# Kernel tuning notes

Hardware: AMD Instinct MI355X
Metric: run time of the kernel (lower is better)

Reference implementation:

```python
import jax, jax.numpy as jnp
import numpy as np

D_MODEL, D_STATE, D_CONV, EXPAND = 1024, 128, 4, 2
D_INNER = D_MODEL * EXPAND
PROJ_DIM = 2 * D_INNER + 2 * D_STATE + 1
CLIP = 8.0
EPS = 1e-5


def setup_inputs() -> dict:
    key = jax.random.key(0)
    ks = jax.random.split(key, 4)
    B, T = 4, 4096
    x = jax.random.normal(ks[0], (B, T, D_MODEL), dtype=jnp.float32)
    in_proj_w = jax.random.normal(ks[1], (PROJ_DIM, D_MODEL), dtype=jnp.float32) / np.sqrt(D_MODEL)
    conv_w = jax.random.normal(ks[2], (D_INNER, 1, D_CONV), dtype=jnp.float32) / np.sqrt(D_CONV)
    A_log = jnp.log(jnp.arange(1, D_STATE + 1, dtype=jnp.float32))
    Dp = jnp.ones((D_INNER,), jnp.float32)
    norm_w = jnp.ones((D_INNER,), jnp.float32)
    out_proj_w = jax.random.normal(ks[3], (D_MODEL, D_INNER), dtype=jnp.float32) / np.sqrt(D_INNER)
    return {"x": x, "in_proj_w": in_proj_w, "conv_w": conv_w, "A_log": A_log,
            "Dp": Dp, "norm_w": norm_w, "out_proj_w": out_proj_w}


def _csilu(v):
    return jnp.minimum(jax.nn.silu(v), CLIP)


def reference(x, in_proj_w, conv_w, A_log, Dp, norm_w, out_proj_w):
    B, T, _ = x.shape
    zxbcdt = x @ in_proj_w.T                                  # (B,T,PROJ_DIM)
    z = zxbcdt[..., :D_INNER]
    xm = zxbcdt[..., D_INNER:2 * D_INNER]
    Bp = zxbcdt[..., 2 * D_INNER:2 * D_INNER + D_STATE]
    Cp = zxbcdt[..., 2 * D_INNER + D_STATE:2 * D_INNER + 2 * D_STATE]
    dt = zxbcdt[..., -1]                                      # (B,T)

    xm = _csilu(xm)
    # causal depthwise conv1d (left pad d_conv-1, valid conv)
    xc = jnp.swapaxes(xm, 1, 2)                               # (B,D_INNER,T)
    xc = jnp.pad(xc, ((0, 0), (0, 0), (D_CONV - 1, 0)))
    xc = jax.lax.conv_general_dilated(
        xc, conv_w, window_strides=(1,), padding='VALID',
        dimension_numbers=('NCH', 'OIH', 'NCH'), feature_group_count=D_INNER)
    xm = _csilu(jnp.swapaxes(xc, 1, 2))                       # (B,T,D_INNER)

    A = -jnp.exp(A_log)                                       # (S,)
    dts = jax.nn.softplus(dt)                                 # (B,T)
    A_bar = jnp.exp(A[None, None, :] * dts[:, :, None])       # (B,T,S)
    B_bar = Bp * dts[:, :, None]                              # (B,T,S)

    h0 = jnp.zeros((B, D_INNER, D_STATE), x.dtype)

    def step(h, inp):
        a, b, c, xt = inp                                     # a,b,c:(B,S)  xt:(B,D_INNER)
        h = a[:, None, :] * h + b[:, None, :] * xt[:, :, None]
        y = jnp.einsum('bds,bs->bd', h, c) + Dp * xt
        return h, y

    xs = (jnp.swapaxes(A_bar, 0, 1), jnp.swapaxes(B_bar, 0, 1),
          jnp.swapaxes(Cp, 0, 1), jnp.swapaxes(xm, 0, 1))
    hT, ys = jax.lax.scan(step, h0, xs)
    y = jnp.swapaxes(ys, 0, 1)                                # (B,T,D_INNER)

    # RMSNorm then gate
    y = y * jax.lax.rsqrt(jnp.mean(y * y, axis=-1, keepdims=True) + EPS) * norm_w
    y = y * _csilu(z)
    out = y @ out_proj_w.T                                    # (B,T,D_MODEL)
    return out, jax.lax.stop_gradient(hT)
```

## Files before the change

kernel.cpp:

```cpp
#include <hip/hip_runtime.h>
#include <hip/hip_bf16.h>
#include <math.h>
#include <stdint.h>

#define D_MODEL 1024
#define D_STATE 128
#define D_INNER 2048
#define NCOLS   4352
#define NB      4
#define TLEN    4096
#define BT      16384
#define LCH     512
#define NCH     8

using bf16 = __hip_bfloat16;
typedef __attribute__((ext_vector_type(2))) float f32x2;
typedef __attribute__((ext_vector_type(4))) float f32x4;
typedef __attribute__((ext_vector_type(8))) short short8x;

__device__ __forceinline__ float csilu_fast(float v) {
    float e = __expf(-v);
    float s = v * __builtin_amdgcn_rcpf(1.f + e);
    return fminf(s, 8.f);
}

__device__ __forceinline__ void gload_lds16(const void* g, void* l) {
    __builtin_amdgcn_global_load_lds(
        (const __attribute__((address_space(1))) void*)g,
        (__attribute__((address_space(3))) void*)l, 16, 0, 0);
}

__global__ __launch_bounds__(256) void cast_kernel(const float* __restrict__ src,
                                                   bf16* __restrict__ dst, int n4) {
    int i = blockIdx.x * 256 + threadIdx.x;
    if (i < n4) {
        float4 v = ((const float4*)src)[i];
        dst[i*4+0] = __float2bfloat16(v.x);
        dst[i*4+1] = __float2bfloat16(v.y);
        dst[i*4+2] = __float2bfloat16(v.z);
        dst[i*4+3] = __float2bfloat16(v.w);
    }
}

__global__ __launch_bounds__(256) void split_kernel(const float* __restrict__ src,
                                                    bf16* __restrict__ hi,
                                                    bf16* __restrict__ lo, int n4) {
    int i = blockIdx.x * 256 + threadIdx.x;
    if (i < n4) {
        float4 v = ((const float4*)src)[i];
        #pragma unroll
        for (int j = 0; j < 4; ++j) {
            float f = (&v.x)[j];
            bf16 h = __float2bfloat16(f);
            hi[i*4+j] = h;
            lo[i*4+j] = __float2bfloat16(f - __bfloat162float(h));
        }
    }
}

__global__ __launch_bounds__(256) void gemm1_split(const bf16* __restrict__ Ah,
                                                   const bf16* __restrict__ Al,
                                                   const bf16* __restrict__ Bh,
                                                   const bf16* __restrict__ Bl,
                                                   bf16* __restrict__ zdst,
                                                   float* __restrict__ xmdst,
                                                   float* __restrict__ bcdst) {
    const int K = D_MODEL;
    __shared__ __align__(16) bf16 sAh[128*32], sAl[128*32];
    __shared__ __align__(16) bf16 sBh[128*32], sBl[128*32];
    const int tid  = threadIdx.x;
    const int lane = tid & 63;
    const int wave = tid >> 6;
    const int wr   = (wave >> 1) * 64;
    const int wc   = (wave & 1) * 64;
    const long arow0 = (long)blockIdx.x * 128;
    const long brow0 = (long)blockIdx.y * 128;
    const long kb = (long)K * 2;
    const bool prec = (blockIdx.y >= 16);
    const char* gAh = (const char*)Ah;
    const char* gAl = (const char*)Al;
    const char* gBh = (const char*)Bh;
    const char* gBl = (const char*)Bl;

    f32x4 acc[4][4] = {};
    const int c1 = tid, c2 = tid + 256;
    const long aoff1 = (arow0 + (c1 >> 2)) * kb + (c1 & 3) * 16;
    const long aoff2 = (arow0 + (c2 >> 2)) * kb + (c2 & 3) * 16;
    const long boff1 = (brow0 + (c1 >> 2)) * kb + (c1 & 3) * 16;
    const long boff2 = (brow0 + (c2 >> 2)) * kb + (c2 & 3) * 16;

    for (int k0 = 0; k0 < K; k0 += 32) {
        __syncthreads();
        const long kk = (long)k0 * 2;
        gload_lds16(gAh + aoff1 + kk, (char*)sAh + c1*16);
        gload_lds16(gAh + aoff2 + kk, (char*)sAh + c2*16);
        gload_lds16(gBh + boff1 + kk, (char*)sBh + c1*16);
        gload_lds16(gBh + boff2 + kk, (char*)sBh + c2*16);
        if (prec) {
            gload_lds16(gAl + aoff1 + kk, (char*)sAl + c1*16);
            gload_lds16(gAl + aoff2 + kk, (char*)sAl + c2*16);
            gload_lds16(gBl + boff1 + kk, (char*)sBl + c1*16);
            gload_lds16(gBl + boff2 + kk, (char*)sBl + c2*16);
        }
        __syncthreads();

        const int r    = lane & 15;
        const int koff = (lane >> 4) * 8;
        short8x ah[4], bh[4];
        #pragma unroll
        for (int m = 0; m < 4; ++m)
            ah[m] = *(const short8x*)(sAh + (wr + m*16 + r) * 32 + koff);
        #pragma unroll
        for (int n = 0; n < 4; ++n)
            bh[n] = *(const short8x*)(sBh + (wc + n*16 + r) * 32 + koff);
        if (prec) {
            short8x al[4], bl[4];
            #pragma unroll
            for (int m = 0; m < 4; ++m)
                al[m] = *(const short8x*)(sAl + (wr + m*16 + r) * 32 + koff);
            #pragma unroll
            for (int n = 0; n < 4; ++n)
                bl[n] = *(const short8x*)(sBl + (wc + n*16 + r) * 32 + koff);
            #pragma unroll
            for (int m = 0; m < 4; ++m)
                #pragma unroll
                for (int n = 0; n < 4; ++n) {
                    acc[m][n] = __builtin_amdgcn_mfma_f32_16x16x32_bf16(ah[m], bh[n], acc[m][n], 0, 0, 0);
                    acc[m][n] = __builtin_amdgcn_mfma_f32_16x16x32_bf16(ah[m], bl[n], acc[m][n], 0, 0, 0);
                    acc[m][n] = __builtin_amdgcn_mfma_f32_16x16x32_bf16(al[m], bh[n], acc[m][n], 0, 0, 0);
                }
        } else {
            #pragma unroll
            for (int m = 0; m < 4; ++m)
                #pragma unroll
                for (int n = 0; n < 4; ++n)
                    acc[m][n] = __builtin_amdgcn_mfma_f32_16x16x32_bf16(ah[m], bh[n], acc[m][n], 0, 0, 0);
        }
    }

    const int r4 = (lane >> 4) * 4;
    const int cl = lane & 15;
    if (blockIdx.y < 16) {
        #pragma unroll
        for (int m = 0; m < 4; ++m)
            #pragma unroll
            for (int n = 0; n < 4; ++n) {
                const long row = arow0 + wr + m*16 + r4;
                const long col = brow0 + wc + n*16 + cl;
                #pragma unroll
                for (int j = 0; j < 4; ++j)
                    zdst[(row + j) * 2048 + col] = __float2bfloat16(acc[m][n][j]);
            }
    } else if (blockIdx.y < 32) {
        #pragma unroll
        for (int m = 0; m < 4; ++m)
            #pragma unroll
            for (int n = 0; n < 4; ++n) {
                const long row = arow0 + wr + m*16 + r4;
                const long col = brow0 - 2048 + wc + n*16 + cl;
                #pragma unroll
                for (int j = 0; j < 4; ++j)
                    xmdst[(row + j) * 2048 + col] = acc[m][n][j];
            }
    } else {
        #pragma unroll
        for (int m = 0; m < 4; ++m)
            #pragma unroll
            for (int n = 0; n < 4; ++n) {
                const long row = arow0 + wr + m*16 + r4;
                const long col = brow0 - 4096 + wc + n*16 + cl;
                #pragma unroll
                for (int j = 0; j < 4; ++j)
                    bcdst[(row + j) * 256 + col] = acc[m][n][j];
            }
    }
}

__global__ __launch_bounds__(256) void gemm2_mfma(const bf16* __restrict__ A,
                                                  const bf16* __restrict__ B,
                                                  float* __restrict__ C) {
    const int K = D_INNER;
    __shared__ __align__(16) bf16 sA[128*32];
    __shared__ __align__(16) bf16 sB[128*32];
    const int tid  = threadIdx.x;
    const int lane = tid & 63;
    const int wave = tid >> 6;
    const int wr   = (wave >> 1) * 64;
    const int wc   = (wave & 1) * 64;
    const long arow0 = (long)blockIdx.x * 128;
    const long brow0 = (long)blockIdx.y * 128;
    const long kb = (long)K * 2;
    const char* gA = (const char*)A;
    const char* gB = (const char*)B;

    f32x4 acc[4][4] = {};
    const int c1 = tid, c2 = tid + 256;
    for (int k0 = 0; k0 < K; k0 += 32) {
        __syncthreads();
        gload_lds16(gA + (arow0 + (c1 >> 2)) * kb + k0*2 + (c1 & 3) * 16, (char*)sA + c1*16);
        gload_lds16(gA + (arow0 + (c2 >> 2)) * kb + k0*2 + (c2 & 3) * 16, (char*)sA + c2*16);
        gload_lds16(gB + (brow0 + (c1 >> 2)) * kb + k0*2 + (c1 & 3) * 16, (char*)sB + c1*16);
        gload_lds16(gB + (brow0 + (c2 >> 2)) * kb + k0*2 + (c2 & 3) * 16, (char*)sB + c2*16);
        __syncthreads();

        const int r    = lane & 15;
        const int koff = (lane >> 4) * 8;
        short8x af[4], bfr[4];
        #pragma unroll
        for (int m = 0; m < 4; ++m)
            af[m] = *(const short8x*)(sA + (wr + m*16 + r) * 32 + koff);
        #pragma unroll
        for (int n = 0; n < 4; ++n)
            bfr[n] = *(const short8x*)(sB + (wc + n*16 + r) * 32 + koff);
        #pragma unroll
        for (int m = 0; m < 4; ++m)
            #pragma unroll
            for (int n = 0; n < 4; ++n)
                acc[m][n] = __builtin_amdgcn_mfma_f32_16x16x32_bf16(af[m], bfr[n], acc[m][n], 0, 0, 0);
    }

    const int r4 = (lane >> 4) * 4;
    const int cl = lane & 15;
    #pragma unroll
    for (int m = 0; m < 4; ++m) {
        #pragma unroll
        for (int n = 0; n < 4; ++n) {
            const long row = arow0 + wr + m*16 + r4;
            const long col = brow0 + wc + n*16 + cl;
            #pragma unroll
            for (int j = 0; j < 4; ++j)
                C[(row + j) * D_MODEL + col] = acc[m][n][j];
        }
    }
}

__global__ __launch_bounds__(256) void dt_gemv(const float* __restrict__ x,
                                               const float* __restrict__ wdt,
                                               float* __restrict__ dts) {
    const int row  = blockIdx.x * 4 + (threadIdx.x >> 6);
    const int lane = threadIdx.x & 63;
    const float4* xr = (const float4*)(x + (long)row * D_MODEL);
    const float4* wr = (const float4*)wdt;
    float acc = 0.f;
    for (int i = lane; i < D_MODEL/4; i += 64) {
        float4 a = xr[i], b = wr[i];
        acc += a.x*b.x + a.y*b.y + a.z*b.z + a.w*b.w;
    }
    for (int o = 32; o > 0; o >>= 1) acc += __shfl_down(acc, o);
    if (lane == 0)
        dts[row] = fmaxf(acc, 0.f) + log1pf(expf(-fabsf(acc)));
}

__global__ __launch_bounds__(LCH) void cumsum_chunks(const float* __restrict__ dts,
                                                     float* __restrict__ cumdt) {
    __shared__ float s[LCH];
    const int t = threadIdx.x;
    const long base = (long)blockIdx.x * LCH;
    s[t] = dts[base + t];
    __syncthreads();
    for (int o = 1; o < LCH; o <<= 1) {
        float v = (t >= o) ? s[t - o] : 0.f;
        __syncthreads();
        s[t] += v;
        __syncthreads();
    }
    cumdt[base + t] = s[t];
}

__global__ __launch_bounds__(256) void scan_local(const float* __restrict__ dts,
                                                  const float* __restrict__ bc,
                                                  const float* __restrict__ A_log,
                                                  const float* __restrict__ xm,
                                                  const float* __restrict__ cw,
                                                  const float* __restrict__ Dp,
                                                  bf16* __restrict__ ybuf,
                                                  float* __restrict__ hbuf) {
    const int tid = threadIdx.x;
    const int dl  = tid & 63;
    const int q   = tid >> 6;
    const int d0  = blockIdx.x * 128 + dl;
    const int d1  = d0 + 64;
    const int ch  = blockIdx.y;
    const int b   = blockIdx.z;
    const long row0 = (long)b * TLEN + ch * LCH;
    const int s0   = q * 32;
    const int scol = dl & 31;
    const int half = dl >> 5;
    const int sg   = s0 + scol;
    const float As_l = -expf(A_log[sg]);

    const float w00 = cw[d0*4+0], w01 = cw[d0*4+1], w02 = cw[d0*4+2], w03 = cw[d0*4+3];
    const float w10 = cw[d1*4+0], w11 = cw[d1*4+1], w12 = cw[d1*4+2], w13 = cw[d1*4+3];
    const float dpv0 = Dp[d0], dpv1 = Dp[d1];

    float p00 = 0.f, p01 = 0.f, p02 = 0.f;
    float p10 = 0.f, p11 = 0.f, p12 = 0.f;
    if (ch != 0) {
        p00 = csilu_fast(xm[(row0 - 3) * 2048 + d0]);
        p01 = csilu_fast(xm[(row0 - 2) * 2048 + d0]);
        p02 = csilu_fast(xm[(row0 - 1) * 2048 + d0]);
        p10 = csilu_fast(xm[(row0 - 3) * 2048 + d1]);
        p11 = csilu_fast(xm[(row0 - 2) * 2048 + d1]);
        p12 = csilu_fast(xm[(row0 - 1) * 2048 + d1]);
    }

    f32x2 hA[16], hB[16];
    #pragma unroll
    for (int k = 0; k < 16; ++k) { hA[k] = (f32x2){0.f,0.f}; hB[k] = (f32x2){0.f,0.f}; }

    __shared__ __align__(16) float sa[8][128], sb[8][128], sc[8][128];
    __shared__ __align__(16) f32x2 yred[2][8][4][64];
    int pbuf = 0;

    float pfDT[4], pfB[4], pfC[4], pfXM0[8], pfXM1[8];
    #pragma unroll
    for (int k = 0; k < 4; ++k) {
        const long row = row0 + half + k*2;
        pfDT[k] = dts[row];
        pfB[k]  = bc[row*256 + sg];
        pfC[k]  = bc[row*256 + 128 + sg];
    }
    #pragma unroll
    for (int r = 0; r < 8; ++r) {
        pfXM0[r] = xm[(row0 + r) * 2048 + d0];
        pfXM1[r] = xm[(row0 + r) * 2048 + d1];
    }

    for (int tt = 0; tt < LCH; tt += 8) {
        #pragma unroll
        for (int k = 0; k < 4; ++k) {
            const int r = half + k*2;
            sa[r][sg] = __expf(As_l * pfDT[k]);
            sb[r][sg] = pfB[k] * pfDT[k];
            sc[r][sg] = pfC[k];
        }
        float curXM0[8], curXM1[8];
        #pragma unroll
        for (int r = 0; r < 8; ++r) { curXM0[r] = pfXM0[r]; curXM1[r] = pfXM1[r]; }
        if (tt + 8 < LCH) {
            #pragma unroll
            for (int k = 0; k < 4; ++k) {
                const long row = row0 + tt + 8 + half + k*2;
                pfDT[k] = dts[row];
                pfB[k]  = bc[row*256 + sg];
                pfC[k]  = bc[row*256 + 128 + sg];
            }
            #pragma unroll
            for (int r = 0; r < 8; ++r) {
                pfXM0[r] = xm[(row0 + tt + 8 + r) * 2048 + d0];
                pfXM1[r] = xm[(row0 + tt + 8 + r) * 2048 + d1];
            }
        }
        #pragma unroll
        for (int r = 0; r < 8; ++r) {
            const float cur0 = csilu_fast(curXM0[r]);
            const float cur1 = csilu_fast(curXM1[r]);
            const float xc0  = csilu_fast(w00*p00 + w01*p01 + w02*p02 + w03*cur0);
            const float xc1  = csilu_fast(w10*p10 + w11*p11 + w12*p12 + w13*cur1);
            p00 = p01; p01 = p02; p02 = cur0;
            p10 = p11; p11 = p12; p12 = cur1;
            const f32x2 x0 = (f32x2){xc0, xc0};
            const f32x2 x1 = (f32x2){xc1, xc1};
            f32x2 yA0 = {0.f,0.f}, yB0 = {0.f,0.f};
            f32x2 yA1 = {0.f,0.f}, yB1 = {0.f,0.f};
            #pragma unroll
            for (int k = 0; k < 8; ++k) {
                const f32x4 a4 = *(const f32x4*)&sa[r][s0 + k*4];
                const f32x4 b4 = *(const f32x4*)&sb[r][s0 + k*4];
                const f32x4 c4 = *(const f32x4*)&sc[r][s0 + k*4];
                const f32x2 aL = {a4.x, a4.y}, aH = {a4.z, a4.w};
                const f32x2 bL = {b4.x, b4.y}, bH = {b4.z, b4.w};
                const f32x2 cL = {c4.x, c4.y}, cH = {c4.z, c4.w};
                hA[k*2+0] = aL * hA[k*2+0] + bL * x0;
                hA[k*2+1] = aH * hA[k*2+1] + bH * x0;
                hB[k*2+0] = aL * hB[k*2+0] + bL * x1;
                hB[k*2+1] = aH * hB[k*2+1] + bH * x1;
                yA0 = hA[k*2+0] * cL + yA0;
                yB0 = hA[k*2+1] * cH + yB0;
                yA1 = hB[k*2+0] * cL + yA1;
                yB1 = hB[k*2+1] * cH + yB1;
            }
            f32x2 ypair;
            ypair.x = (yA0.x + yA0.y) + (yB0.x + yB0.y) + (q == 0 ? dpv0 * xc0 : 0.f);
            ypair.y = (yA1.x + yA1.y) + (yB1.x + yB1.y) + (q == 0 ? dpv1 * xc1 : 0.f);
            yred[pbuf][r][q][dl] = ypair;
        }
        __syncthreads();
        #pragma unroll
        for (int i2 = 0; i2 < 4; ++i2) {
            const int i = tid + i2 * 256;
            const int r = i >> 7, c = i & 127;
            const int cl2 = c & 63;
            float y = 0.f;
            if (c < 64) {
                #pragma unroll
                for (int q2 = 0; q2 < 4; ++q2) y += yred[pbuf][r][q2][cl2].x;
            } else {
                #pragma unroll
                for (int q2 = 0; q2 < 4; ++q2) y += yred[pbuf][r][q2][cl2].y;
            }
            ybuf[(row0 + tt + r) * 2048 + blockIdx.x * 128 + c] = __float2bfloat16(y);
        }
        pbuf ^= 1;
    }
    const long hb0 = ((long)(b * NCH + ch) * 2048 + d0) * 128;
    const long hb1 = ((long)(b * NCH + ch) * 2048 + d1) * 128;
    #pragma unroll
    for (int k = 0; k < 8; ++k) {
        *(float4*)&hbuf[hb0 + s0 + k*4] = make_float4(hA[k*2].x, hA[k*2].y, hA[k*2+1].x, hA[k*2+1].y);
        *(float4*)&hbuf[hb1 + s0 + k*4] = make_float4(hB[k*2].x, hB[k*2].y, hB[k*2+1].x, hB[k*2+1].y);
    }
}

__global__ __launch_bounds__(256) void scan_comb(const float* __restrict__ hbuf,
                                                 const float* __restrict__ cumdt,
                                                 const float* __restrict__ A_log,
                                                 bf16* __restrict__ hinH,
                                                 bf16* __restrict__ hinL,
                                                 float* __restrict__ hT) {
    const long idx = (long)blockIdx.x * 256 + threadIdx.x;
    const int s = (int)(idx & 127);
    const int d = (int)((idx >> 7) & 2047);
    const int b = (int)(idx >> 18);
    const float As = -expf(A_log[s]);
    float hr = 0.f;
    for (int c = 0; c < NCH; ++c) {
        const long off = ((long)(b * NCH + c) * 2048 + d) * 128 + s;
        const float loc = hbuf[off];
        const bf16 hh = __float2bfloat16(hr);
        hinH[off] = hh;
        hinL[off] = __float2bfloat16(hr - __bfloat162float(hh));
        const float p = __expf(As * cumdt[(long)b * TLEN + c * LCH + (LCH - 1)]);
        hr = p * hr + loc;
    }
    hT[((long)b * 2048 + d) * 128 + s] = hr;
}

__global__ __launch_bounds__(256) void cmod_build(const float* __restrict__ cumdt,
                                                  const float* __restrict__ bc,
                                                  const float* __restrict__ A_log,
                                                  bf16* __restrict__ cmod) {
    const long i = (long)blockIdx.x * 256 + threadIdx.x;
    const int s = (int)(i & 127);
    const long row = i >> 7;
    const float As = -__expf(A_log[s]);
    cmod[i] = __float2bfloat16(bc[row*256 + 128 + s] * __expf(As * cumdt[row]));
}

__global__ __launch_bounds__(256) void corr_gemm(const bf16* __restrict__ cmod,
                                                 const bf16* __restrict__ hinH,
                                                 const bf16* __restrict__ hinL,
                                                 bf16* __restrict__ ybuf) {
    __shared__ __align__(16) bf16 sA[128*32];
    __shared__ __align__(16) bf16 sBh[128*32], sBl[128*32];
    const int tid  = threadIdx.x;
    const int lane = tid & 63;
    const int wave = tid >> 6;
    const int wr   = (wave >> 1) * 64;
    const int wc   = (wave & 1) * 64;
    const long arow0 = (long)blockIdx.x * 128;
    const long bcol0 = (long)blockIdx.y * 128;
    const int b  = (int)(arow0 >> 12);
    const int ch = (int)((arow0 & 4095) >> 9);
    const char* gA = (const char*)cmod;
    const char* gH = (const char*)(hinH + (long)(b * NCH + ch) * 2048 * 128);
    const char* gL = (const char*)(hinL + (long)(b * NCH + ch) * 2048 * 128);

    f32x4 acc[4][4] = {};
    const int c1 = tid, c2 = tid + 256;
    for (int k0 = 0; k0 < 128; k0 += 32) {
        __syncthreads();
        gload_lds16(gA + (arow0 + (c1 >> 2))*256 + k0*2 + (c1 & 3)*16, (char*)sA + c1*16);
        gload_lds16(gA + (arow0 + (c2 >> 2))*256 + k0*2 + (c2 & 3)*16, (char*)sA + c2*16);
        gload_lds16(gH + (bcol0 + (c1 >> 2))*256 + k0*2 + (c1 & 3)*16, (char*)sBh + c1*16);
        gload_lds16(gH + (bcol0 + (c2 >> 2))*256 + k0*2 + (c2 & 3)*16, (char*)sBh + c2*16);
        gload_lds16(gL + (bcol0 + (c1 >> 2))*256 + k0*2 + (c1 & 3)*16, (char*)sBl + c1*16);
        gload_lds16(gL + (bcol0 + (c2 >> 2))*256 + k0*2 + (c2 & 3)*16, (char*)sBl + c2*16);
        __syncthreads();

        const int r    = lane & 15;
        const int koff = (lane >> 4) * 8;
        short8x af[4], bh[4], bl[4];
        #pragma unroll
        for (int m = 0; m < 4; ++m)
            af[m] = *(const short8x*)(sA + (wr + m*16 + r) * 32 + koff);
        #pragma unroll
        for (int n = 0; n < 4; ++n) {
            bh[n] = *(const short8x*)(sBh + (wc + n*16 + r) * 32 + koff);
            bl[n] = *(const short8x*)(sBl + (wc + n*16 + r) * 32 + koff);
        }
        #pragma unroll
        for (int m = 0; m < 4; ++m)
            #pragma unroll
            for (int n = 0; n < 4; ++n) {
                acc[m][n] = __builtin_amdgcn_mfma_f32_16x16x32_bf16(af[m], bh[n], acc[m][n], 0, 0, 0);
                acc[m][n] = __builtin_amdgcn_mfma_f32_16x16x32_bf16(af[m], bl[n], acc[m][n], 0, 0, 0);
            }
    }

    const int r4 = (lane >> 4) * 4;
    const int cl = lane & 15;
    #pragma unroll
    for (int m = 0; m < 4; ++m) {
        #pragma unroll
        for (int n = 0; n < 4; ++n) {
            const long row = arow0 + wr + m*16 + r4;
            const long col = bcol0 + wc + n*16 + cl;
            #pragma unroll
            for (int j = 0; j < 4; ++j) {
                const long o = (row + j) * 2048 + col;
                ybuf[o] = __float2bfloat16(__bfloat162float(ybuf[o]) + acc[m][n][j]);
            }
        }
    }
}

__global__ __launch_bounds__(256) void rms_z(const bf16* __restrict__ ybuf,
                                             bf16* __restrict__ zg,
                                             const float* __restrict__ norm_w) {
    const long row = blockIdx.x;
    const int tid = threadIdx.x;
    float v[8];
    float ss = 0.f;
    #pragma unroll
    for (int i = 0; i < 8; ++i) {
        v[i] = __bfloat162float(ybuf[row * D_INNER + i*256 + tid]);
        ss += v[i] * v[i];
    }
    __shared__ float red[256];
    red[tid] = ss;
    __syncthreads();
    for (int o = 128; o > 0; o >>= 1) {
        if (tid < o) red[tid] += red[tid + o];
        __syncthreads();
    }
    const float scale = rsqrtf(red[0] * (1.f / D_INNER) + 1e-5f);
    #pragma unroll
    for (int i = 0; i < 8; ++i) {
        const int dd = i*256 + tid;
        const float z = __bfloat162float(zg[row * D_INNER + dd]);
        zg[row * D_INNER + dd] = __float2bfloat16(v[i] * scale * norm_w[dd] * csilu_fast(z));
    }
}

extern "C" void kernel_launch(void* const* d_in, const int* in_sizes, int n_in,
                              void* d_out, int out_size, void* d_ws, size_t ws_size,
                              hipStream_t stream) {
    const float* x      = (const float*)d_in[0];
    const float* in_w   = (const float*)d_in[1];
    const float* conv_w = (const float*)d_in[2];
    const float* A_log  = (const float*)d_in[3];
    const float* Dp     = (const float*)d_in[4];
    const float* norm_w = (const float*)d_in[5];
    const float* out_w  = (const float*)d_in[6];
    float* out = (float*)d_out;
    float* hT  = out + (long)BT * D_MODEL;

    char* ws = (char*)d_ws;
    size_t off = 0;
    auto alloc = [&](size_t bytes) { void* p = ws + off; off += (bytes + 255) & ~(size_t)255; return p; };
    bf16*  zg    = (bf16*) alloc((size_t)BT * D_INNER * 2);
    float* xm    = (float*)alloc((size_t)BT * D_INNER * 4);
    float* bcbuf = (float*)alloc((size_t)BT * 256 * 4);
    bf16*  w2b   = (bf16*) alloc((size_t)D_MODEL * D_INNER * 2);
    float* hbuf  = (float*)alloc((size_t)NB * NCH * 128 * D_INNER * 4);
    float* dts   = (float*)alloc((size_t)BT * 4);
    float* cumdt = (float*)alloc((size_t)BT * 4);
    if (ws_size < off) return;

    bf16* whi = (bf16*)hbuf;
    bf16* wlo = whi + (size_t)NCOLS * D_MODEL;
    bf16* xhi = (bf16*)d_out;
    bf16* xlo = xhi + (size_t)BT * D_MODEL;
    bf16* ybuf = (bf16*)d_out;
    bf16* hinH = (bf16*)xm;
    bf16* hinL = hinH + (size_t)NB * NCH * D_INNER * 128;
    bf16* cmod = hinL + (size_t)NB * NCH * D_INNER * 128;

    split_kernel<<<BT*D_MODEL/4/256, 256, 0, stream>>>(x, xhi, xlo, BT*D_MODEL/4);
    split_kernel<<<NCOLS*D_MODEL/4/256, 256, 0, stream>>>(in_w, whi, wlo, NCOLS*D_MODEL/4);
    cast_kernel<<<D_MODEL*D_INNER/4/256, 256, 0, stream>>>(out_w, w2b, D_MODEL*D_INNER/4);

    gemm1_split<<<dim3(BT/128, NCOLS/128), 256, 0, stream>>>(xhi, xlo, whi, wlo, zg, xm, bcbuf);
    dt_gemv<<<BT/4, 256, 0, stream>>>(x, in_w + (long)NCOLS * D_MODEL, dts);
    cumsum_chunks<<<NB*NCH, LCH, 0, stream>>>(dts, cumdt);
    scan_local<<<dim3(D_INNER/128, NCH, NB), 256, 0, stream>>>(dts, bcbuf, A_log, xm, conv_w, Dp, ybuf, hbuf);
    scan_comb<<<NB*128*D_INNER/256, 256, 0, stream>>>(hbuf, cumdt, A_log, hinH, hinL, hT);
    cmod_build<<<BT*128/256, 256, 0, stream>>>(cumdt, bcbuf, A_log, cmod);
    corr_gemm<<<dim3(BT/128, D_INNER/128), 256, 0, stream>>>(cmod, hinH, hinL, ybuf);
    rms_z<<<BT, 256, 0, stream>>>(ybuf, zg, norm_w);
    gemm2_mfma<<<dim3(BT/128, D_MODEL/128), 256, 0, stream>>>(zg, w2b, out);
}
```

Measured before the change: 1.052 ms.

## Split conv+silu across warps via shared memory and defer y reduction one step

Each of the four wavefronts previously recomputed the causal conv and clipped SiLU for all 8 timesteps redundantly. Now each wavefront computes 2 timesteps, using a 5-row window of xm loads, and writes them to a double-buffered shared array. The cross-wavefront y reduction for step tt-8 is moved after the barrier of step tt, so one __syncthreads per iteration covers both, with a tail flush after the loop. This cuts redundant exp/rcp work and xm loads, but puts a shared-memory round trip on the recurrence input path.

Measured after the change: 1.003 ms, median of 2. -4.7%, faster.

```diff
diff --git a/kernel.cpp b/kernel.cpp
--- a/kernel.cpp
+++ b/kernel.cpp
@@ -293,26 +293,16 @@
     const float w10 = cw[d1*4+0], w11 = cw[d1*4+1], w12 = cw[d1*4+2], w13 = cw[d1*4+3];
     const float dpv0 = Dp[d0], dpv1 = Dp[d1];
 
-    float p00 = 0.f, p01 = 0.f, p02 = 0.f;
-    float p10 = 0.f, p11 = 0.f, p12 = 0.f;
-    if (ch != 0) {
-        p00 = csilu_fast(xm[(row0 - 3) * 2048 + d0]);
-        p01 = csilu_fast(xm[(row0 - 2) * 2048 + d0]);
-        p02 = csilu_fast(xm[(row0 - 1) * 2048 + d0]);
-        p10 = csilu_fast(xm[(row0 - 3) * 2048 + d1]);
-        p11 = csilu_fast(xm[(row0 - 2) * 2048 + d1]);
-        p12 = csilu_fast(xm[(row0 - 1) * 2048 + d1]);
-    }
-
     f32x2 hA[16], hB[16];
     #pragma unroll
     for (int k = 0; k < 16; ++k) { hA[k] = (f32x2){0.f,0.f}; hB[k] = (f32x2){0.f,0.f}; }
 
     __shared__ __align__(16) float sa[8][128], sb[8][128], sc[8][128];
+    __shared__ __align__(16) float sxc[2][8][128];
     __shared__ __align__(16) f32x2 yred[2][8][4][64];
     int pbuf = 0;
 
-    float pfDT[4], pfB[4], pfC[4], pfXM0[8], pfXM1[8];
+    float pfDT[4], pfB[4], pfC[4], pfX0[5], pfX1[5];
     #pragma unroll
     for (int k = 0; k < 4; ++k) {
         const long row = row0 + half + k*2;
@@ -321,9 +311,11 @@
         pfC[k]  = bc[row*256 + 128 + sg];
     }
     #pragma unroll
-    for (int r = 0; r < 8; ++r) {
-        pfXM0[r] = xm[(row0 + r) * 2048 + d0];
-        pfXM1[r] = xm[(row0 + r) * 2048 + d1];
+    for (int j = 0; j < 5; ++j) {
+        const int t = 2*q - 3 + j;
+        const bool ok = (ch != 0) || (t >= 0);
+        pfX0[j] = ok ? xm[(row0 + t) * 2048 + d0] : 0.f;
+        pfX1[j] = ok ? xm[(row0 + t) * 2048 + d1] : 0.f;
     }
 
     for (int tt = 0; tt < LCH; tt += 8) {
@@ -334,9 +326,15 @@
             sb[r][sg] = pfB[k] * pfDT[k];
             sc[r][sg] = pfC[k];
         }
-        float curXM0[8], curXM1[8];
-        #pragma unroll
-        for (int r = 0; r < 8; ++r) { curXM0[r] = pfXM0[r]; curXM1[r] = pfXM1[r]; }
+        {
+            float px0[5], px1[5];
+            #pragma unroll
+            for (int j = 0; j < 5; ++j) { px0[j] = csilu_fast(pfX0[j]); px1[j] = csilu_fast(pfX1[j]); }
+            sxc[pbuf][2*q+0][dl]      = csilu_fast(w00*px0[0] + w01*px0[1] + w02*px0[2] + w03*px0[3]);
+            sxc[pbuf][2*q+1][dl]      = csilu_fast(w00*px0[1] + w01*px0[2] + w02*px0[3] + w03*px0[4]);
+            sxc[pbuf][2*q+0][dl+64]   = csilu_fast(w10*px1[0] + w11*px1[1] + w12*px1[2] + w13*px1[3]);
+            sxc[pbuf][2*q+1][dl+64]   = csilu_fast(w10*px1[1] + w11*px1[2] + w12*px1[3] + w13*px1[4]);
+        }
         if (tt + 8 < LCH) {
             #pragma unroll
             for (int k = 0; k < 4; ++k) {
@@ -345,20 +343,35 @@
                 pfB[k]  = bc[row*256 + sg];
                 pfC[k]  = bc[row*256 + 128 + sg];
             }
-            #pragma unroll
-            for (int r = 0; r < 8; ++r) {
-                pfXM0[r] = xm[(row0 + tt + 8 + r) * 2048 + d0];
-                pfXM1[r] = xm[(row0 + tt + 8 + r) * 2048 + d1];
+            const int tr = tt + 8 + 2*q;
+            #pragma unroll
+            for (int j = 0; j < 5; ++j) {
+                pfX0[j] = xm[(row0 + tr - 3 + j) * 2048 + d0];
+                pfX1[j] = xm[(row0 + tr - 3 + j) * 2048 + d1];
+            }
+        }
+        __syncthreads();
+        if (tt > 0) {
+            #pragma unroll
+            for (int i2 = 0; i2 < 4; ++i2) {
+                const int i = tid + i2 * 256;
+                const int r = i >> 7, c = i & 127;
+                const int cl2 = c & 63;
+                float y = 0.f;
+                if (c < 64) {
+                    #pragma unroll
+                    for (int q2 = 0; q2 < 4; ++q2) y += yred[pbuf^1][r][q2][cl2].x;
+                } else {
+                    #pragma unroll
+                    for (int q2 = 0; q2 < 4; ++q2) y += yred[pbuf^1][r][q2][cl2].y;
+                }
+                ybuf[(row0 + (tt-8) + r) * 2048 + blockIdx.x * 128 + c] = __float2bfloat16(y);
             }
         }
         #pragma unroll
         for (int r = 0; r < 8; ++r) {
-            const float cur0 = csilu_fast(curXM0[r]);
-            const float cur1 = csilu_fast(curXM1[r]);
-            const float xc0  = csilu_fast(w00*p00 + w01*p01 + w02*p02 + w03*cur0);
-            const float xc1  = csilu_fast(w10*p10 + w11*p11 + w12*p12 + w13*cur1);
-            p00 = p01; p01 = p02; p02 = cur0;
-            p10 = p11; p11 = p12; p12 = cur1;
+            const float xc0 = sxc[pbuf][r][dl];
+            const float xc1 = sxc[pbuf][r][dl+64];
             const f32x2 x0 = (f32x2){xc0, xc0};
             const f32x2 x1 = (f32x2){xc1, xc1};
             f32x2 yA0 = {0.f,0.f}, yB0 = {0.f,0.f};
@@ -385,23 +398,23 @@
             ypair.y = (yA1.x + yA1.y) + (yB1.x + yB1.y) + (q == 0 ? dpv1 * xc1 : 0.f);
             yred[pbuf][r][q][dl] = ypair;
         }
-        __syncthreads();
-        #pragma unroll
-        for (int i2 = 0; i2 < 4; ++i2) {
-            const int i = tid + i2 * 256;
-            const int r = i >> 7, c = i & 127;
-            const int cl2 = c & 63;
-            float y = 0.f;
-            if (c < 64) {
-                #pragma unroll
-                for (int q2 = 0; q2 < 4; ++q2) y += yred[pbuf][r][q2][cl2].x;
-            } else {
-                #pragma unroll
-                for (int q2 = 0; q2 < 4; ++q2) y += yred[pbuf][r][q2][cl2].y;
-            }
-            ybuf[(row0 + tt + r) * 2048 + blockIdx.x * 128 + c] = __float2bfloat16(y);
-        }
         pbuf ^= 1;
+    }
+    __syncthreads();
+    #pragma unroll
+    for (int i2 = 0; i2 < 4; ++i2) {
+        const int i = tid + i2 * 256;
+        const int r = i >> 7, c = i & 127;
+        const int cl2 = c & 63;
+        float y = 0.f;
+        if (c < 64) {
+            #pragma unroll
+            for (int q2 = 0; q2 < 4; ++q2) y += yred[pbuf^1][r][q2][cl2].x;
+        } else {
+            #pragma unroll
+            for (int q2 = 0; q2 < 4; ++q2) y += yred[pbuf^1][r][q2][cl2].y;
+        }
+        ybuf[(row0 + (LCH-8) + r) * 2048 + blockIdx.x * 128 + c] = __float2bfloat16(y);
     }
     const long hb0 = ((long)(b * NCH + ch) * 2048 + d0) * 128;
     const long hb1 = ((long)(b * NCH + ch) * 2048 + d1) * 128;
```
